# Optimization experiments

Measured on AMD Instinct MI355X. Metric: run time of the kernel, lower is better.

Reference implementation:

```python
import jax, jax.numpy as jnp
import numpy as np
from jax import lax

B, Z, X, Y = 8, 4, 32, 32
N = Z * X * Y
REAL_SIZE = jnp.array([25.0, 25.0, 4.0], dtype=jnp.float32)
THRESHOLD = 0.5
CUTOFF = 2.0


def setup_inputs() -> dict:
    key = jax.random.key(0)
    k1, k2 = jax.random.split(key)
    pred = jax.random.normal(k1, (B, Z, X, Y, 10), dtype=jnp.float32)
    targ = jax.random.uniform(k2, (B, Z, X, Y, 10), dtype=jnp.float32)
    return {"pred": pred, "targ": targ}


def _grid():
    z, x, y = jnp.meshgrid(jnp.arange(Z), jnp.arange(X), jnp.arange(Y), indexing="ij")
    return jnp.stack([z, x, y], -1).reshape(N, 3).astype(jnp.float32)


def _nms_mask(adj0, a0):
    # Fixed-size masked version of the original iterative suppression:
    # adj0: [N,N] bool, strictly-upper-triangular 'closer than cutoff' graph
    # a0:   [N] bool, currently active (above-threshold) points in conf-desc order
    def step(state):
        a, _ = state
        m = adj0 & a[:, None] & a[None, :]
        mf = m.astype(jnp.float32)
        r = mf.sum(0)                              # restrain_tensor = DIS.sum(0)
        r = r - (r != 0).astype(jnp.float32) @ mf  # subtract suppressed suppressors
        return ((r == 0.0) & a, a.sum())
    def cond(state):
        a, prev = state
        return a.sum() != prev
    a, _ = lax.while_loop(cond, step, (a0, jnp.int32(-1)))
    return a


def _per_batch(pd_conf, pd_pos, pd_R, tg_conf, tg_pos, tg_R):
    # pd_conf/tg_conf: [N]; pd_pos/tg_pos: [N,3] normalized; pd_R/tg_R: [N,3,3]
    pd_active = pd_conf > THRESHOLD
    tg_active = tg_conf > THRESHOLD
    # sort predictions by confidence descending, inactive pushed to the end
    skey = jnp.where(pd_active, pd_conf, -jnp.inf)
    order = jnp.argsort(-skey)
    pd_pos = pd_pos[order]
    pd_R = pd_R[order]
    a0 = pd_active[order]
    # NMS in NORMALIZED coordinates (as in the original module: real_size scaling
    # is applied only AFTER argnms)
    d = jnp.sqrt(jnp.sum((pd_pos[:, None, :] - pd_pos[None, :, :]) ** 2, -1))  # [N,N]
    iu = jnp.arange(N)
    adj0 = (d < CUTOFF) & (iu[:, None] < iu[None, :])
    keep = lax.stop_gradient(_nms_mask(adj0, a0))
    # greedy matching in real coordinates
    pd_r = pd_pos * REAL_SIZE
    tg_r = tg_pos * REAL_SIZE
    dist = jnp.sqrt(jnp.sum((tg_r[:, None, :] - pd_r[None, :, :]) ** 2, -1))  # [N_tg, N_pd]
    within = (dist < CUTOFF) & tg_active[:, None] & keep[None, :]
    has = within.any(0)                 # pred j has at least one target within cutoff
    first_tg = jnp.argmax(within, 0)    # first (lowest-index) matching target per pred
    tp = has.sum().astype(jnp.int32)
    n_pd = keep.sum().astype(jnp.int32)
    n_tg = tg_active.sum().astype(jnp.int32)
    cm = jnp.stack([tp, n_pd - tp, n_tg - tp])  # [matched, unmatched_pred, unmatched_targ]
    # mean rotation-angle error over matched pairs (3 rotation rows each)
    tgRm = tg_R[first_tg]  # [N,3,3]
    cos = jnp.sum(pd_R * tgRm, -1) / (
        jnp.linalg.norm(pd_R, axis=-1) * jnp.linalg.norm(tgRm, axis=-1))
    ang = jnp.arccos(jnp.clip(cos, -1.0, 1.0)) / jnp.pi * 180.0  # [N,3]
    w = has.astype(jnp.float32)[:, None]
    ms = jnp.where(tp > 0,
                   jnp.sum(ang * w) / (3.0 * jnp.maximum(tp, 1).astype(jnp.float32)),
                   0.0)
    return cm, ms


def _forward(pred, targ):
    grid = _grid()
    zxy = jnp.array([Z, X, Y], dtype=jnp.float32)
    def fields(t, is_pred):
        conf = jax.nn.sigmoid(t[..., 0]) if is_pred else t[..., 0]
        conf = conf.reshape(B, N)
        pos = (t[..., 1:4].reshape(B, N, 3) + grid) / zxy  # (off + cell_idx)/ZXY
        rx = t[..., 4:7].reshape(B, N, 3)
        ry = t[..., 7:10].reshape(B, N, 3)
        R = jnp.stack([rx, ry, jnp.cross(rx, ry)], axis=-2)  # [B,N,3,3]
        return conf, pos, R
    pc, pp, pR = fields(pred, True)
    tc, tpos, tR = fields(targ, False)
    cm, ms = jax.vmap(_per_batch)(pc, pp, pR, tc, tpos, tR)
    return cm.reshape(B, 1, 1, 3), ms.reshape(B, 1, 1, 1).astype(jnp.float32)


def reference(pred, targ):
    return _forward(pred, targ)
```

## Files before the change

### kernel.cpp

```cpp
#include <hip/hip_runtime.h>
#include <math.h>

#define NB    8
#define NPTS  4096
#define NTH   1024
#define SPT   4
#define NFILT 16
#define MAXQ  512
#define MAXU  256
#define MAXK  256

#define WS_PCC  0
#define WS_TCC  512
#define WS_PKEY 1024
#define WS_PPOS 263168
#define WS_TPOS 787456

__device__ __forceinline__ int blockReduceSumI(int v, int* scr, int tid) {
    #pragma unroll
    for (int o = 32; o > 0; o >>= 1) v += __shfl_down(v, o, 64);
    if ((tid & 63) == 0) scr[tid >> 6] = v;
    __syncthreads();
    if (tid == 0) {
        int s = 0;
        #pragma unroll
        for (int w = 0; w < NTH / 64; ++w) s += scr[w];
        scr[16] = s;
    }
    __syncthreads();
    return scr[16];
}

__device__ __forceinline__ float blockReduceSumF(float v, float* scr, int tid) {
    #pragma unroll
    for (int o = 32; o > 0; o >>= 1) v += __shfl_down(v, o, 64);
    if ((tid & 63) == 0) scr[tid >> 6] = v;
    __syncthreads();
    if (tid == 0) {
        float s = 0.0f;
        #pragma unroll
        for (int w = 0; w < NTH / 64; ++w) s += scr[w];
        scr[16] = s;
    }
    __syncthreads();
    return scr[16];
}

__device__ __forceinline__ float rowAngleDeg(float a0, float a1, float a2,
                                             float b0, float b1, float b2) {
    float dot = a0 * b0 + a1 * b1 + a2 * b2;
    float na = sqrtf(a0 * a0 + a1 * a1 + a2 * a2);
    float nb = sqrtf(b0 * b0 + b1 * b1 + b2 * b2);
    float c = dot / (na * nb);
    c = fminf(1.0f, fmaxf(-1.0f, c));
    return acosf(c) * 57.29577951308232f;
}

__global__ __launch_bounds__(256) void prep_kernel(const float* __restrict__ pred,
                                                   const float* __restrict__ targ,
                                                   unsigned char* __restrict__ ws) {
    __shared__ int wcnt[4];
    unsigned int* pcc = (unsigned int*)(ws + WS_PCC);
    unsigned int* tcc = (unsigned int*)(ws + WS_TCC);
    unsigned long long* pkey = (unsigned long long*)(ws + WS_PKEY);
    float4* ppos = (float4*)(ws + WS_PPOS);
    float4* tpos = (float4*)(ws + WS_TPOS);

    const int tid = threadIdx.x;
    const int blk = blockIdx.x;
    const int tensor = blk >> 7;
    const int batch = (blk >> 4) & 7;
    const int chunk = blk & 15;
    const int n = chunk * 256 + tid;
    const float* base = (tensor ? targ : pred)
                        + (size_t)batch * NPTS * 10 + (size_t)n * 10;
    float2 f0 = *(const float2*)base;
    float2 f1 = *(const float2*)(base + 2);
    float gz = (float)(n >> 10);
    float gx = (float)((n >> 5) & 31);
    float gy = (float)(n & 31);

    bool active;
    unsigned long long key = 0;
    float4 rec;
    if (tensor == 0) {
        float conf = 1.0f / (1.0f + expf(-f0.x));
        active = conf > 0.5f;
        unsigned int u = ~(__float_as_uint(conf) | 0x80000000u);
        key = ((unsigned long long)u << 32) | (unsigned int)n;
        rec = make_float4((f0.y + gz) * 0.25f,
                          (f1.x + gx) * 0.03125f,
                          (f1.y + gy) * 0.03125f,
                          (float)n);
    } else {
        active = f0.x > 0.5f;
        rec = make_float4((f0.y + gz) * 0.25f * 25.0f,
                          (f1.x + gx) * 0.03125f * 25.0f,
                          (f1.y + gy) * 0.03125f * 4.0f,
                          (float)n);
    }

    const int lane = tid & 63, wid = tid >> 6;
    unsigned long long ball = __ballot(active);
    int lofs = __popcll(ball & ((1ull << lane) - 1ull));
    if (lane == 0) wcnt[wid] = __popcll(ball);
    __syncthreads();
    int wb = 0;
    for (int w = 0; w < wid; ++w) wb += wcnt[w];
    if (tid == 0) {
        unsigned int t = (unsigned int)(wcnt[0] + wcnt[1] + wcnt[2] + wcnt[3]);
        (tensor ? tcc : pcc)[batch * 16 + chunk] = t;
    }
    if (active) {
        int e = batch * NPTS + chunk * 256 + wb + lofs;
        if (tensor == 0) { pkey[e] = key; ppos[e] = rec; }
        else tpos[e] = rec;
    }
}

__global__ __launch_bounds__(NTH) void molan_kernel(const float* __restrict__ pred,
                                                    const float* __restrict__ targ,
                                                    const unsigned char* __restrict__ ws,
                                                    float* __restrict__ out) {
    __shared__ int   scr_i[32];
    __shared__ float scr_f[32];
    __shared__ int   cnt[4];
    __shared__ int   ccP[16], ccT[16];
    __shared__ unsigned long long f_key[NFILT];
    __shared__ float f_x[NFILT], f_y[NFILT], f_z[NFILT];
    __shared__ unsigned long long q_key[MAXQ];
    __shared__ float q_x[MAXQ], q_y[MAXQ], q_z[MAXQ];
    __shared__ int   q_res[MAXQ];
    __shared__ unsigned long long u_key[MAXU];
    __shared__ float u_x[MAXU], u_y[MAXU], u_z[MAXU];
    __shared__ float k_x[MAXK], k_y[MAXK], k_z[MAXK];
    __shared__ int   k_idx[MAXK];
    __shared__ unsigned int k_match[MAXK];

    const int b = blockIdx.x;
    const int tid = threadIdx.x;
    const float* pb = pred + (size_t)b * NPTS * 10;
    const float* tb = targ + (size_t)b * NPTS * 10;
    const unsigned long long* pkey = (const unsigned long long*)(ws + WS_PKEY) + b * NPTS;
    const float4* ppos = (const float4*)(ws + WS_PPOS) + b * NPTS;
    const float4* tpos = (const float4*)(ws + WS_TPOS) + b * NPTS;

    if (tid < 16) ccP[tid] = (int)((const unsigned int*)(ws + WS_PCC))[b * 16 + tid];
    else if (tid < 32) ccT[tid - 16] = (int)((const unsigned int*)(ws + WS_TCC))[b * 16 + tid - 16];
    __syncthreads();

    unsigned long long key[SPT];
    bool  act[SPT];
    int   pidx[SPT];
    float cx[SPT], cy[SPT], cz[SPT];
    #pragma unroll
    for (int s = 0; s < SPT; ++s) {
        int slot = tid + NTH * s;
        bool a = (slot & 255) < ccP[slot >> 8];
        act[s] = a;
        key[s] = ~0ull;
        cx[s] = cy[s] = cz[s] = 0.f; pidx[s] = 0;
        if (a) {
            key[s] = pkey[slot];
            float4 p = ppos[slot];
            cx[s] = p.x; cy[s] = p.y; cz[s] = p.z; pidx[s] = (int)p.w;
        }
    }
    bool  t_act[SPT];
    int   t_n[SPT];
    float t_x[SPT], t_y[SPT], t_z[SPT];
    #pragma unroll
    for (int s = 0; s < SPT; ++s) {
        int slot = tid + NTH * s;
        bool a = (slot & 255) < ccT[slot >> 8];
        t_act[s] = a;
        t_x[s] = t_y[s] = t_z[s] = 0.f; t_n[s] = 0;
        if (a) {
            float4 p = tpos[slot];
            t_x[s] = p.x; t_y[s] = p.y; t_z[s] = p.z; t_n[s] = (int)p.w;
        }
    }

    int loc = 0;
    #pragma unroll
    for (int s = 0; s < SPT; ++s) loc += act[s] ? 1 : 0;
    int cur = blockReduceSumI(loc, scr_i, tid);
    int prev = -1;
    while (cur != prev) {
        {
            unsigned long long bk = ~0ull;
            float bx = 0.f, by = 0.f, bz = 0.f;
            #pragma unroll
            for (int s = 0; s < SPT; ++s)
                if (act[s] && key[s] < bk) { bk = key[s]; bx = cx[s]; by = cy[s]; bz = cz[s]; }
            #pragma unroll
            for (int o = 32; o > 0; o >>= 1) {
                unsigned long long ok = __shfl_xor(bk, o, 64);
                float ox = __shfl_xor(bx, o, 64);
                float oy = __shfl_xor(by, o, 64);
                float oz = __shfl_xor(bz, o, 64);
                if (ok < bk) { bk = ok; bx = ox; by = oy; bz = oz; }
            }
            if ((tid & 63) == 0) {
                int w = tid >> 6;
                f_key[w] = bk; f_x[w] = bx; f_y[w] = by; f_z[w] = bz;
            }
        }
        __syncthreads();

        bool sflag[SPT], pend[SPT];
        #pragma unroll
        for (int s = 0; s < SPT; ++s) {
            sflag[s] = false; pend[s] = false;
            if (!act[s]) continue;
            bool found = false;
            for (int f = 0; f < NFILT; ++f) {
                if (f_key[f] < key[s]) {
                    float dx = f_x[f] - cx[s], dy = f_y[f] - cy[s], dz = f_z[f] - cz[s];
                    if (dx * dx + dy * dy + dz * dz < 4.0f) { found = true; break; }
                }
            }
            if (found) sflag[s] = true;
            else pend[s] = true;
        }
        do {
            if (tid == 0) cnt[1] = 0;
            __syncthreads();
            int qe[SPT];
            #pragma unroll
            for (int s = 0; s < SPT; ++s) {
                qe[s] = -1;
                if (pend[s]) {
                    int e = atomicAdd(&cnt[1], 1);
                    if (e < MAXQ) {
                        q_key[e] = key[s]; q_x[e] = cx[s]; q_y[e] = cy[s]; q_z[e] = cz[s];
                        q_res[e] = 0;
                        qe[s] = e; pend[s] = false;
                    }
                }
            }
            __syncthreads();
            const int Q = min(cnt[1], MAXQ);
            for (int e = 0; e < Q; ++e) {
                unsigned long long qk = q_key[e];
                float qx = q_x[e], qy = q_y[e], qz = q_z[e];
                bool hit = false;
                #pragma unroll
                for (int s = 0; s < SPT; ++s) {
                    if (act[s] && key[s] < qk) {
                        float dx = cx[s] - qx, dy = cy[s] - qy, dz = cz[s] - qz;
                        if (dx * dx + dy * dy + dz * dz < 4.0f) hit = true;
                    }
                }
                if (hit) q_res[e] = 1;
            }
            __syncthreads();
            #pragma unroll
            for (int s = 0; s < SPT; ++s)
                if (qe[s] >= 0) sflag[s] = (q_res[qe[s]] != 0);
        } while (cnt[1] > MAXQ);

        bool upend[SPT], supp[SPT];
        #pragma unroll
        for (int s = 0; s < SPT; ++s) {
            upend[s] = act[s] && !sflag[s];
            supp[s] = false;
        }
        do {
            if (tid == 0) cnt[2] = 0;
            __syncthreads();
            #pragma unroll
            for (int s = 0; s < SPT; ++s) {
                if (upend[s]) {
                    int e = atomicAdd(&cnt[2], 1);
                    if (e < MAXU) {
                        u_key[e] = key[s]; u_x[e] = cx[s]; u_y[e] = cy[s]; u_z[e] = cz[s];
                        upend[s] = false;
                    }
                }
            }
            __syncthreads();
            const int Ku = min(cnt[2], MAXU);
            #pragma unroll
            for (int s = 0; s < SPT; ++s) {
                if (!act[s] || supp[s]) continue;
                for (int e = 0; e < Ku; ++e) {
                    if (u_key[e] < key[s]) {
                        float dx = u_x[e] - cx[s], dy = u_y[e] - cy[s], dz = u_z[e] - cz[s];
                        if (dx * dx + dy * dy + dz * dz < 4.0f) { supp[s] = true; break; }
                    }
                }
            }
        } while (cnt[2] > MAXU);
        loc = 0;
        #pragma unroll
        for (int s = 0; s < SPT; ++s) {
            if (act[s] && supp[s]) act[s] = false;
            loc += act[s] ? 1 : 0;
        }
        prev = cur;
        cur = blockReduceSumI(loc, scr_i, tid);
    }
    const int n_pd = cur;

    bool kpend[SPT];
    #pragma unroll
    for (int s = 0; s < SPT; ++s) kpend[s] = act[s];
    int loc_tp = 0;
    float loc_ang = 0.0f;
    do {
        if (tid == 0) cnt[3] = 0;
        __syncthreads();
        #pragma unroll
        for (int s = 0; s < SPT; ++s) {
            if (kpend[s]) {
                int e = atomicAdd(&cnt[3], 1);
                if (e < MAXK) {
                    k_x[e] = cx[s] * 25.0f; k_y[e] = cy[s] * 25.0f; k_z[e] = cz[s] * 4.0f;
                    k_idx[e] = pidx[s];
                    k_match[e] = 0xFFFFFFFFu;
                    kpend[s] = false;
                }
            }
        }
        __syncthreads();
        const int K = min(cnt[3], MAXK);
        #pragma unroll
        for (int s = 0; s < SPT; ++s) {
            if (!t_act[s]) continue;
            float tx = t_x[s], ty = t_y[s], tz = t_z[s];
            for (int e = 0; e < K; ++e) {
                float dx = tx - k_x[e], dy = ty - k_y[e], dz = tz - k_z[e];
                if (dx * dx + dy * dy + dz * dz < 4.0f)
                    atomicMin(&k_match[e], (unsigned int)t_n[s]);
            }
        }
        __syncthreads();
        if (tid < K) {
            unsigned int m = k_match[tid];
            if (m != 0xFFFFFFFFu) {
                ++loc_tp;
                const float2* pr = (const float2*)(pb + (size_t)k_idx[tid] * 10 + 4);
                float2 p0 = pr[0], p1 = pr[1], p2v = pr[2];
                float ax0 = p0.x, ax1 = p0.y, ax2 = p1.x;
                float ay0 = p1.y, ay1 = p2v.x, ay2 = p2v.y;
                float az0 = ax1 * ay2 - ax2 * ay1;
                float az1 = ax2 * ay0 - ax0 * ay2;
                float az2 = ax0 * ay1 - ax1 * ay0;
                const float2* tr = (const float2*)(tb + (size_t)m * 10 + 4);
                float2 t0 = tr[0], t1 = tr[1], t2v = tr[2];
                float bx0 = t0.x, bx1 = t0.y, bx2 = t1.x;
                float by0 = t1.y, by1 = t2v.x, by2 = t2v.y;
                float bz0 = bx1 * by2 - bx2 * by1;
                float bz1 = bx2 * by0 - bx0 * by2;
                float bz2 = bx0 * by1 - bx1 * by0;
                loc_ang += rowAngleDeg(ax0, ax1, ax2, bx0, bx1, bx2);
                loc_ang += rowAngleDeg(ay0, ay1, ay2, by0, by1, by2);
                loc_ang += rowAngleDeg(az0, az1, az2, bz0, bz1, bz2);
            }
        }
    } while (cnt[3] > MAXK);

    int tp = blockReduceSumI(loc_tp, scr_i, tid);
    float angsum = blockReduceSumF(loc_ang, scr_f, tid);

    if (tid == 0) {
        int nt = 0;
        #pragma unroll
        for (int i = 0; i < 16; ++i) nt += ccT[i];
        out[b * 3 + 0] = (float)tp;
        out[b * 3 + 1] = (float)(n_pd - tp);
        out[b * 3 + 2] = (float)(nt - tp);
        out[NB * 3 + b] = (tp > 0) ? (angsum / (3.0f * (float)tp)) : 0.0f;
    }
}

extern "C" void kernel_launch(void* const* d_in, const int* in_sizes, int n_in,
                              void* d_out, int out_size, void* d_ws, size_t ws_size,
                              hipStream_t stream) {
    const float* pred = (const float*)d_in[0];
    const float* targ = (const float*)d_in[1];
    float* out = (float*)d_out;
    unsigned char* ws = (unsigned char*)d_ws;
    prep_kernel<<<dim3(256), dim3(256), 0, stream>>>(pred, targ, ws);
    molan_kernel<<<dim3(NB), dim3(NTH), 0, stream>>>(pred, targ, ws, out);
}
```

Before: 76.18 us.

## Fuse prep and NMS kernels into one cooperative launch with grid sync

Merges the compaction/prep kernel into the main per-batch kernel, launched cooperatively with 64 blocks of 1024 threads. A grid-wide sync separates the prep phase from the per-batch NMS and matching phase, after which only 8 blocks continue. This removes one kernel launch and the gap between the two launches, at the cost of grid-sync overhead and fewer, larger blocks in the prep phase. The initial active count now comes from the per-chunk counts, replacing a block reduction.

```diff
diff --git a/kernel.cpp b/kernel.cpp
--- a/kernel.cpp
+++ b/kernel.cpp
@@ -1,5 +1,8 @@
 #include <hip/hip_runtime.h>
+#include <hip/hip_cooperative_groups.h>
 #include <math.h>
+
+namespace cg = cooperative_groups;
 
 #define NB    8
 #define NPTS  4096
@@ -56,72 +59,11 @@
     return acosf(c) * 57.29577951308232f;
 }
 
-__global__ __launch_bounds__(256) void prep_kernel(const float* __restrict__ pred,
-                                                   const float* __restrict__ targ,
-                                                   unsigned char* __restrict__ ws) {
-    __shared__ int wcnt[4];
-    unsigned int* pcc = (unsigned int*)(ws + WS_PCC);
-    unsigned int* tcc = (unsigned int*)(ws + WS_TCC);
-    unsigned long long* pkey = (unsigned long long*)(ws + WS_PKEY);
-    float4* ppos = (float4*)(ws + WS_PPOS);
-    float4* tpos = (float4*)(ws + WS_TPOS);
-
-    const int tid = threadIdx.x;
-    const int blk = blockIdx.x;
-    const int tensor = blk >> 7;
-    const int batch = (blk >> 4) & 7;
-    const int chunk = blk & 15;
-    const int n = chunk * 256 + tid;
-    const float* base = (tensor ? targ : pred)
-                        + (size_t)batch * NPTS * 10 + (size_t)n * 10;
-    float2 f0 = *(const float2*)base;
-    float2 f1 = *(const float2*)(base + 2);
-    float gz = (float)(n >> 10);
-    float gx = (float)((n >> 5) & 31);
-    float gy = (float)(n & 31);
-
-    bool active;
-    unsigned long long key = 0;
-    float4 rec;
-    if (tensor == 0) {
-        float conf = 1.0f / (1.0f + expf(-f0.x));
-        active = conf > 0.5f;
-        unsigned int u = ~(__float_as_uint(conf) | 0x80000000u);
-        key = ((unsigned long long)u << 32) | (unsigned int)n;
-        rec = make_float4((f0.y + gz) * 0.25f,
-                          (f1.x + gx) * 0.03125f,
-                          (f1.y + gy) * 0.03125f,
-                          (float)n);
-    } else {
-        active = f0.x > 0.5f;
-        rec = make_float4((f0.y + gz) * 0.25f * 25.0f,
-                          (f1.x + gx) * 0.03125f * 25.0f,
-                          (f1.y + gy) * 0.03125f * 4.0f,
-                          (float)n);
-    }
-
-    const int lane = tid & 63, wid = tid >> 6;
-    unsigned long long ball = __ballot(active);
-    int lofs = __popcll(ball & ((1ull << lane) - 1ull));
-    if (lane == 0) wcnt[wid] = __popcll(ball);
-    __syncthreads();
-    int wb = 0;
-    for (int w = 0; w < wid; ++w) wb += wcnt[w];
-    if (tid == 0) {
-        unsigned int t = (unsigned int)(wcnt[0] + wcnt[1] + wcnt[2] + wcnt[3]);
-        (tensor ? tcc : pcc)[batch * 16 + chunk] = t;
-    }
-    if (active) {
-        int e = batch * NPTS + chunk * 256 + wb + lofs;
-        if (tensor == 0) { pkey[e] = key; ppos[e] = rec; }
-        else tpos[e] = rec;
-    }
-}
-
-__global__ __launch_bounds__(NTH) void molan_kernel(const float* __restrict__ pred,
+__global__ __launch_bounds__(NTH) void fused_kernel(const float* __restrict__ pred,
                                                     const float* __restrict__ targ,
-                                                    const unsigned char* __restrict__ ws,
+                                                    unsigned char* __restrict__ ws,
                                                     float* __restrict__ out) {
+    __shared__ int   wcnt16[16];
     __shared__ int   scr_i[32];
     __shared__ float scr_f[32];
     __shared__ int   cnt[4];
@@ -137,8 +79,71 @@
     __shared__ int   k_idx[MAXK];
     __shared__ unsigned int k_match[MAXK];
 
-    const int b = blockIdx.x;
+    const int blk = blockIdx.x;
     const int tid = threadIdx.x;
+
+    {
+        const int tensor = blk >> 5;
+        const int batch = (blk >> 2) & 7;
+        const int n = (blk & 3) * 1024 + tid;
+        const float* base = (tensor ? targ : pred)
+                            + (size_t)batch * NPTS * 10 + (size_t)n * 10;
+        float2 f0 = *(const float2*)base;
+        float2 f1 = *(const float2*)(base + 2);
+        float gz = (float)(n >> 10);
+        float gx = (float)((n >> 5) & 31);
+        float gy = (float)(n & 31);
+
+        bool active;
+        unsigned long long key = 0;
+        float4 rec;
+        if (tensor == 0) {
+            float conf = 1.0f / (1.0f + expf(-f0.x));
+            active = conf > 0.5f;
+            unsigned int u = ~(__float_as_uint(conf) | 0x80000000u);
+            key = ((unsigned long long)u << 32) | (unsigned int)n;
+            rec = make_float4((f0.y + gz) * 0.25f,
+                              (f1.x + gx) * 0.03125f,
+                              (f1.y + gy) * 0.03125f,
+                              (float)n);
+        } else {
+            active = f0.x > 0.5f;
+            rec = make_float4((f0.y + gz) * 0.25f * 25.0f,
+                              (f1.x + gx) * 0.03125f * 25.0f,
+                              (f1.y + gy) * 0.03125f * 4.0f,
+                              (float)n);
+        }
+
+        const int lane = tid & 63, wv = tid >> 6;
+        unsigned long long ball = __ballot(active);
+        int lofs = __popcll(ball & ((1ull << lane) - 1ull));
+        if (lane == 0) wcnt16[wv] = __popcll(ball);
+        __syncthreads();
+        const int group = tid >> 8;
+        int wb = 0;
+        for (int w = group * 4; w < wv; ++w) wb += wcnt16[w];
+        const int chunk256 = (blk & 3) * 4 + group;
+        if ((tid & 255) == 0) {
+            int t = wcnt16[group * 4] + wcnt16[group * 4 + 1]
+                  + wcnt16[group * 4 + 2] + wcnt16[group * 4 + 3];
+            ((unsigned int*)(ws + (tensor ? WS_TCC : WS_PCC)))[batch * 16 + chunk256]
+                = (unsigned int)t;
+        }
+        if (active) {
+            int e = batch * NPTS + chunk256 * 256 + wb + lofs;
+            if (tensor == 0) {
+                ((unsigned long long*)(ws + WS_PKEY))[e] = key;
+                ((float4*)(ws + WS_PPOS))[e] = rec;
+            } else {
+                ((float4*)(ws + WS_TPOS))[e] = rec;
+            }
+        }
+    }
+    __threadfence();
+    cg::this_grid().sync();
+    if (blk >= NB) return;
+
+    const int b = blk;
     const float* pb = pred + (size_t)b * NPTS * 10;
     const float* tb = targ + (size_t)b * NPTS * 10;
     const unsigned long long* pkey = (const unsigned long long*)(ws + WS_PKEY) + b * NPTS;
@@ -148,6 +153,9 @@
     if (tid < 16) ccP[tid] = (int)((const unsigned int*)(ws + WS_PCC))[b * 16 + tid];
     else if (tid < 32) ccT[tid - 16] = (int)((const unsigned int*)(ws + WS_TCC))[b * 16 + tid - 16];
     __syncthreads();
+    int np = 0, nt = 0;
+    #pragma unroll
+    for (int i = 0; i < 16; ++i) { np += ccP[i]; nt += ccT[i]; }
 
     unsigned long long key[SPT];
     bool  act[SPT];
@@ -181,10 +189,7 @@
         }
     }
 
-    int loc = 0;
-    #pragma unroll
-    for (int s = 0; s < SPT; ++s) loc += act[s] ? 1 : 0;
-    int cur = blockReduceSumI(loc, scr_i, tid);
+    int cur = np;
     int prev = -1;
     while (cur != prev) {
         {
@@ -292,7 +297,7 @@
                 }
             }
         } while (cnt[2] > MAXU);
-        loc = 0;
+        int loc = 0;
         #pragma unroll
         for (int s = 0; s < SPT; ++s) {
             if (act[s] && supp[s]) act[s] = false;
@@ -365,9 +370,6 @@
     float angsum = blockReduceSumF(loc_ang, scr_f, tid);
 
     if (tid == 0) {
-        int nt = 0;
-        #pragma unroll
-        for (int i = 0; i < 16; ++i) nt += ccT[i];
         out[b * 3 + 0] = (float)tp;
         out[b * 3 + 1] = (float)(n_pd - tp);
         out[b * 3 + 2] = (float)(nt - tp);
@@ -382,6 +384,7 @@
     const float* targ = (const float*)d_in[1];
     float* out = (float*)d_out;
     unsigned char* ws = (unsigned char*)d_ws;
-    prep_kernel<<<dim3(256), dim3(256), 0, stream>>>(pred, targ, ws);
-    molan_kernel<<<dim3(NB), dim3(NTH), 0, stream>>>(pred, targ, ws, out);
-}
+    void* args[] = {(void*)&pred, (void*)&targ, (void*)&ws, (void*)&out};
+    hipLaunchCooperativeKernel((const void*)fused_kernel, dim3(64), dim3(NTH),
+                               args, 0, stream);
+}
```

Result: slower. 117.6 us (+54.3%).

## Halve block threads, pack prediction records, and fuse final reductions

Applied to the files above, without the earlier changes.

Each per-batch block now runs 512 threads with 8 points per thread instead of 1024 threads with 4, which means fewer waves in every block-wide reduction and barrier of the iterative NMS loop. The prediction key and position are packed into one 32-byte record so each point is read with two adjacent 16-byte loads. The initial active count is taken from the per-chunk counts instead of a block reduction, and the final tp and angle reductions share one barrier pass. The cost is less parallelism per point and more register pressure per thread in a kernel that only launches eight blocks.

```diff
diff --git a/kernel.cpp b/kernel.cpp
--- a/kernel.cpp
+++ b/kernel.cpp
@@ -3,18 +3,18 @@
 
 #define NB    8
 #define NPTS  4096
-#define NTH   1024
-#define SPT   4
-#define NFILT 16
+#define NTH   512
+#define SPT   8
+#define NWAVE (NTH / 64)
+#define NFILT NWAVE
 #define MAXQ  512
 #define MAXU  256
 #define MAXK  256
 
 #define WS_PCC  0
 #define WS_TCC  512
-#define WS_PKEY 1024
-#define WS_PPOS 263168
-#define WS_TPOS 787456
+#define WS_PREC 1024
+#define WS_TPOS 1049600
 
 __device__ __forceinline__ int blockReduceSumI(int v, int* scr, int tid) {
     #pragma unroll
@@ -24,22 +24,7 @@
     if (tid == 0) {
         int s = 0;
         #pragma unroll
-        for (int w = 0; w < NTH / 64; ++w) s += scr[w];
-        scr[16] = s;
-    }
-    __syncthreads();
-    return scr[16];
-}
-
-__device__ __forceinline__ float blockReduceSumF(float v, float* scr, int tid) {
-    #pragma unroll
-    for (int o = 32; o > 0; o >>= 1) v += __shfl_down(v, o, 64);
-    if ((tid & 63) == 0) scr[tid >> 6] = v;
-    __syncthreads();
-    if (tid == 0) {
-        float s = 0.0f;
-        #pragma unroll
-        for (int w = 0; w < NTH / 64; ++w) s += scr[w];
+        for (int w = 0; w < NWAVE; ++w) s += scr[w];
         scr[16] = s;
     }
     __syncthreads();
@@ -62,8 +47,7 @@
     __shared__ int wcnt[4];
     unsigned int* pcc = (unsigned int*)(ws + WS_PCC);
     unsigned int* tcc = (unsigned int*)(ws + WS_TCC);
-    unsigned long long* pkey = (unsigned long long*)(ws + WS_PKEY);
-    float4* ppos = (float4*)(ws + WS_PPOS);
+    ulonglong2* prec = (ulonglong2*)(ws + WS_PREC);
     float4* tpos = (float4*)(ws + WS_TPOS);
 
     const int tid = threadIdx.x;
@@ -82,22 +66,20 @@
 
     bool active;
     unsigned long long key = 0;
-    float4 rec;
+    float rx, ry, rz;
     if (tensor == 0) {
         float conf = 1.0f / (1.0f + expf(-f0.x));
         active = conf > 0.5f;
         unsigned int u = ~(__float_as_uint(conf) | 0x80000000u);
         key = ((unsigned long long)u << 32) | (unsigned int)n;
-        rec = make_float4((f0.y + gz) * 0.25f,
-                          (f1.x + gx) * 0.03125f,
-                          (f1.y + gy) * 0.03125f,
-                          (float)n);
+        rx = (f0.y + gz) * 0.25f;
+        ry = (f1.x + gx) * 0.03125f;
+        rz = (f1.y + gy) * 0.03125f;
     } else {
         active = f0.x > 0.5f;
-        rec = make_float4((f0.y + gz) * 0.25f * 25.0f,
-                          (f1.x + gx) * 0.03125f * 25.0f,
-                          (f1.y + gy) * 0.03125f * 4.0f,
-                          (float)n);
+        rx = (f0.y + gz) * 0.25f * 25.0f;
+        ry = (f1.x + gx) * 0.03125f * 25.0f;
+        rz = (f1.y + gy) * 0.03125f * 4.0f;
     }
 
     const int lane = tid & 63, wid = tid >> 6;
@@ -113,8 +95,16 @@
     }
     if (active) {
         int e = batch * NPTS + chunk * 256 + wb + lofs;
-        if (tensor == 0) { pkey[e] = key; ppos[e] = rec; }
-        else tpos[e] = rec;
+        if (tensor == 0) {
+            unsigned long long xy = ((unsigned long long)__float_as_uint(ry) << 32)
+                                    | __float_as_uint(rx);
+            unsigned long long zn = ((unsigned long long)(unsigned int)n << 32)
+                                    | __float_as_uint(rz);
+            prec[2 * e]     = make_ulonglong2(key, xy);
+            prec[2 * e + 1] = make_ulonglong2(zn, 0ull);
+        } else {
+            tpos[e] = make_float4(rx, ry, rz, (float)n);
+        }
     }
 }
 
@@ -141,13 +131,15 @@
     const int tid = threadIdx.x;
     const float* pb = pred + (size_t)b * NPTS * 10;
     const float* tb = targ + (size_t)b * NPTS * 10;
-    const unsigned long long* pkey = (const unsigned long long*)(ws + WS_PKEY) + b * NPTS;
-    const float4* ppos = (const float4*)(ws + WS_PPOS) + b * NPTS;
+    const ulonglong2* prec = (const ulonglong2*)(ws + WS_PREC) + (size_t)b * NPTS * 2;
     const float4* tpos = (const float4*)(ws + WS_TPOS) + b * NPTS;
 
     if (tid < 16) ccP[tid] = (int)((const unsigned int*)(ws + WS_PCC))[b * 16 + tid];
     else if (tid < 32) ccT[tid - 16] = (int)((const unsigned int*)(ws + WS_TCC))[b * 16 + tid - 16];
     __syncthreads();
+    int np = 0, nt = 0;
+    #pragma unroll
+    for (int i = 0; i < 16; ++i) { np += ccP[i]; nt += ccT[i]; }
 
     unsigned long long key[SPT];
     bool  act[SPT];
@@ -161,9 +153,13 @@
         key[s] = ~0ull;
         cx[s] = cy[s] = cz[s] = 0.f; pidx[s] = 0;
         if (a) {
-            key[s] = pkey[slot];
-            float4 p = ppos[slot];
-            cx[s] = p.x; cy[s] = p.y; cz[s] = p.z; pidx[s] = (int)p.w;
+            ulonglong2 w0 = prec[2 * slot];
+            ulonglong2 w1 = prec[2 * slot + 1];
+            key[s] = w0.x;
+            cx[s] = __uint_as_float((unsigned int)w0.y);
+            cy[s] = __uint_as_float((unsigned int)(w0.y >> 32));
+            cz[s] = __uint_as_float((unsigned int)w1.x);
+            pidx[s] = (int)(w1.x >> 32);
         }
     }
     bool  t_act[SPT];
@@ -181,10 +177,7 @@
         }
     }
 
-    int loc = 0;
-    #pragma unroll
-    for (int s = 0; s < SPT; ++s) loc += act[s] ? 1 : 0;
-    int cur = blockReduceSumI(loc, scr_i, tid);
+    int cur = np;
     int prev = -1;
     while (cur != prev) {
         {
@@ -292,7 +285,7 @@
                 }
             }
         } while (cnt[2] > MAXU);
-        loc = 0;
+        int loc = 0;
         #pragma unroll
         for (int s = 0; s < SPT; ++s) {
             if (act[s] && supp[s]) act[s] = false;
@@ -361,13 +354,17 @@
         }
     } while (cnt[3] > MAXK);
 
-    int tp = blockReduceSumI(loc_tp, scr_i, tid);
-    float angsum = blockReduceSumF(loc_ang, scr_f, tid);
-
+    #pragma unroll
+    for (int o = 32; o > 0; o >>= 1) {
+        loc_tp  += __shfl_down(loc_tp,  o, 64);
+        loc_ang += __shfl_down(loc_ang, o, 64);
+    }
+    if ((tid & 63) == 0) { scr_i[tid >> 6] = loc_tp; scr_f[tid >> 6] = loc_ang; }
+    __syncthreads();
     if (tid == 0) {
-        int nt = 0;
-        #pragma unroll
-        for (int i = 0; i < 16; ++i) nt += ccT[i];
+        int tp = 0; float angsum = 0.0f;
+        #pragma unroll
+        for (int w = 0; w < NWAVE; ++w) { tp += scr_i[w]; angsum += scr_f[w]; }
         out[b * 3 + 0] = (float)tp;
         out[b * 3 + 1] = (float)(n_pd - tp);
         out[b * 3 + 2] = (float)(nt - tp);
```

New measurement: 80.57 us. 1.06x slower.
